# Performance work log

Measured on AMD Instinct MI355X. Metric: run time of the kernel, lower is better.

The kernel has to match this reference:

```python
import jax, jax.numpy as jnp
import numpy as np

N_NODES = 4096
M_NODES = 8192
DIM = 256


def _symnorm(A):
    # D^{-1/2} A D^{-1/2} with eps, via row/col scaling (same math as diag matmuls)
    d = A.sum(axis=1) + 1e-5
    s = d ** -0.5
    return A * s[:, None] * s[None, :]


def _gat(A, X, W, a_src, a_dst, b):
    # Dense-form GATConv (PyG semantics): edges are nonzeros of A plus self loops.
    N = A.shape[0]
    H, F = a_src.shape
    Xp = (X @ W).reshape(N, H, F)                     # [N, H, F]
    src = jnp.einsum('nhf,hf->nh', Xp, a_src)         # score of source node j
    dst = jnp.einsum('nhf,hf->nh', Xp, a_dst)         # score of target node i
    logits = jax.nn.leaky_relu(dst[:, None, :] + src[None, :, :], negative_slope=0.2)  # [i, j, h]
    mask = (A != 0.0) | jnp.eye(N, dtype=bool)        # add_self_loops=True
    logits = jnp.where(mask[:, :, None], logits, -jnp.inf)
    alpha = jax.nn.softmax(logits, axis=1)            # softmax over neighbors j
    out = jnp.einsum('ijh,jhf->ihf', alpha, Xp).reshape(N, H * F) + b
    return out


def setup_inputs() -> dict:
    key = jax.random.key(0)
    ks = jax.random.split(key, 32)

    def p(i, shape, scale=0.05):
        return jax.random.normal(ks[i], shape, dtype=jnp.float32) * scale

    R = jax.random.normal(ks[0], (N_NODES, N_NODES), dtype=jnp.float32)
    A = jax.nn.relu((R + R.T) * 0.5)
    X = jax.random.normal(ks[1], (N_NODES, DIM), dtype=jnp.float32)
    return dict(
        A=A, X=X,
        # down GT0: GATConv(256, 128, heads=4) -> 512
        Wd0=p(2, (256, 512)), asd0=p(3, (4, 128)), add0=p(4, (4, 128)), bd0=p(5, (512,)),
        # down GT1: GATConv(512, 256, heads=4) -> 1024
        Wd1=p(6, (512, 1024)), asd1=p(7, (4, 256)), add1=p(8, (4, 256)), bd1=p(9, (1024,)),
        # pool projections (Linear(in, 1))
        wp0=p(10, (1, 512)), bp0=p(11, (1,)),
        wp1=p(12, (1, 1024)), bp1=p(13, (1,)),
        # bottom GT: GATConv(1024, 512, heads=2) -> 1024
        Wb=p(14, (1024, 1024)), asb=p(15, (2, 512)), adb=p(16, (2, 512)), bb=p(17, (1024,)),
        # up GT (reversed[0]): GATConv(1024, 128, heads=4) -> 512
        Wu0=p(18, (1024, 512)), asu0=p(19, (4, 128)), adu0=p(20, (4, 128)), bu0=p(21, (512,)),
        # up GT (reversed[1]): GATConv(512, 64, heads=4) -> 256
        Wu1=p(22, (512, 256)), asu1=p(23, (4, 64)), adu1=p(24, (4, 64)), bu1=p(25, (256,)),
        # upsampler Linear(n_nodes, m_nodes)
        Wup=p(26, (M_NODES, N_NODES)), bup=p(27, (M_NODES,)),
    )


def reference(A, X, Wd0, asd0, add0, bd0, Wd1, asd1, add1, bd1, wp0, bp0, wp1, bp1,
              Wb, asb, adb, bb, Wu0, asu0, adu0, bu0, Wu1, asu1, adu1, bu1, Wup, bup):
    N0 = A.shape[0]
    A0 = A + jnp.eye(N0, dtype=A.dtype)  # A_ = A + I (used throughout; normalized A is dead code)

    # ---- down level 0 ----
    X0 = jax.nn.relu(_gat(A0, X, Wd0, asd0, add0, bd0))            # [4096, 512]
    s0 = jax.nn.sigmoid(X0 @ wp0[0] + bp0[0])
    k0 = max(2, N0 // 2)                                            # int(0.5 * N)
    v0, idx0 = jax.lax.top_k(s0, k0)
    A1 = _symnorm(A0[idx0][:, idx0])                                # [2048, 2048]
    X1in = X0[idx0] * v0[:, None]

    # ---- down level 1 ----
    X1 = jax.nn.relu(_gat(A1, X1in, Wd1, asd1, add1, bd1))          # [2048, 1024]
    s1 = jax.nn.sigmoid(X1 @ wp1[0] + bp1[0])
    k1 = max(2, k0 // 2)
    v1, idx1 = jax.lax.top_k(s1, k1)
    A2 = _symnorm(A1[idx1][:, idx1])                                # [1024, 1024]
    X2in = X1[idx1] * v1[:, None]

    # ---- bottom ----
    Xb = jax.nn.relu(_gat(A2, X2in, Wb, asb, adb, bb))              # [1024, 1024]

    # ---- up level 0: unpool to level-1 graph ----
    h = jnp.zeros((k0, Xb.shape[1]), Xb.dtype).at[idx1].set(Xb)
    Xu0 = jax.nn.relu(_gat(A1, h, Wu0, asu0, adu0, bu0))            # [2048, 512]
    rec0 = jax.nn.relu(Xu0 @ Xu0.T)

    # ---- up level 1: unpool to original graph ----
    h = jnp.zeros((N0, Xu0.shape[1]), Xu0.dtype).at[idx0].set(Xu0)
    Xu1 = jax.nn.relu(_gat(A0, h, Wu1, asu1, adu1, bu1))            # [4096, 256]
    rec1 = jax.nn.relu(Xu1 @ Xu1.T)

    # ---- upsampler: Linear over node dim, softmax over feature dim, reconstruct adjacency ----
    Z = jax.nn.softmax(Wup @ Xu1 + bup[:, None], axis=1)            # [8192, 256]
    A_up = jax.nn.relu(Z @ Z.T)                                     # [8192, 8192]
    return (A_up, A0, A1, rec0, rec1)
```

## Files before the change

kernel.cpp:

```cpp
#include <hip/hip_runtime.h>
#include <math.h>


typedef short bf16x8 __attribute__((ext_vector_type(8)));
typedef float f32x4 __attribute__((ext_vector_type(4)));

static __device__ __forceinline__ float wave_sum64(float v) {
#pragma unroll
  for (int off = 32; off; off >>= 1) v += __shfl_down(v, off);
  return v;
}

static __device__ __forceinline__ unsigned short f2b(float x) {
  unsigned u = __float_as_uint(x);
  unsigned r = (u + 0x7fffu + ((u >> 16) & 1u)) >> 16;
  return (unsigned short)r;
}

static __device__ __forceinline__ float b2f(unsigned short h) {
  return __uint_as_float(((unsigned)h) << 16);
}

__global__ void k_add_eye(const float* __restrict__ A, float* __restrict__ O) {
  size_t i = ((size_t)blockIdx.x * 256 + threadIdx.x) * 4;
  size_t r = i >> 12, c = i & 4095;
  float4 v = *reinterpret_cast<const float4*>(&A[i]);
  if (r >= c && r < c + 4) ((float*)&v)[r - c] += 1.f;
  *reinterpret_cast<float4*>(&O[i]) = v;
}

__global__ void k_fill0(float* __restrict__ p, int n) {
  int stride = gridDim.x * 256;
  for (int i = blockIdx.x * 256 + threadIdx.x; i < n; i += stride) p[i] = 0.f;
}

__global__ void k_split3(const float* __restrict__ S, unsigned short* __restrict__ D,
                         size_t PS, int n) {
  int stride = gridDim.x * 1024;
  for (int i = (blockIdx.x * 256 + threadIdx.x) * 4; i < n; i += stride) {
    float4 v = *reinterpret_cast<const float4*>(&S[i]);
    float xv[4] = {v.x, v.y, v.z, v.w};
    unsigned short o1[4], o2[4], o3[4];
#pragma unroll
    for (int e = 0; e < 4; ++e) {
      float x = xv[e];
      unsigned short a = f2b(x);
      float r1 = x - b2f(a);
      unsigned short b = f2b(r1);
      float r2 = r1 - b2f(b);
      o1[e] = a; o2[e] = b; o3[e] = f2b(r2);
    }
    *reinterpret_cast<uint2*>(&D[i]) = *reinterpret_cast<const uint2*>(o1);
    *reinterpret_cast<uint2*>(&D[PS + i]) = *reinterpret_cast<const uint2*>(o2);
    *reinterpret_cast<uint2*>(&D[2 * PS + i]) = *reinterpret_cast<const uint2*>(o3);
  }
}

__global__ void k_gather_scale_split3(const float* __restrict__ Xs, int Dd,
    const int* __restrict__ idx, const float* __restrict__ v,
    unsigned short* __restrict__ D, size_t PS) {
  int i = blockIdx.y;
  int f = (blockIdx.x * 256 + threadIdx.x) * 4;
  if (f >= Dd) return;
  float vi = v[i];
  float4 x4 = *reinterpret_cast<const float4*>(&Xs[(size_t)idx[i] * Dd + f]);
  float xv[4] = {x4.x * vi, x4.y * vi, x4.z * vi, x4.w * vi};
  unsigned short o1[4], o2[4], o3[4];
#pragma unroll
  for (int e = 0; e < 4; ++e) {
    float x = xv[e];
    unsigned short a = f2b(x);
    float r1 = x - b2f(a);
    unsigned short b = f2b(r1);
    float r2 = r1 - b2f(b);
    o1[e] = a; o2[e] = b; o3[e] = f2b(r2);
  }
  size_t e0 = (size_t)i * Dd + f;
  *reinterpret_cast<uint2*>(&D[e0]) = *reinterpret_cast<const uint2*>(o1);
  *reinterpret_cast<uint2*>(&D[PS + e0]) = *reinterpret_cast<const uint2*>(o2);
  *reinterpret_cast<uint2*>(&D[2 * PS + e0]) = *reinterpret_cast<const uint2*>(o3);
}

__global__ void k_gather_scale_b16(const float* __restrict__ Xs, int Dd,
    const int* __restrict__ idx, const float* __restrict__ v,
    unsigned short* __restrict__ D) {
  int i = blockIdx.y;
  int f = (blockIdx.x * 256 + threadIdx.x) * 4;
  if (f >= Dd) return;
  float vi = v[i];
  float4 x4 = *reinterpret_cast<const float4*>(&Xs[(size_t)idx[i] * Dd + f]);
  unsigned short o[4] = {f2b(x4.x * vi), f2b(x4.y * vi), f2b(x4.z * vi), f2b(x4.w * vi)};
  *reinterpret_cast<uint2*>(&D[(size_t)i * Dd + f]) = *reinterpret_cast<const uint2*>(o);
}

__global__ __launch_bounds__(256) void k_transpose_bf16(const float* __restrict__ S, int ldS,
    unsigned short* __restrict__ D, int R, int Cc) {
  __shared__ unsigned short T[64][72];
  int r0 = blockIdx.y << 6, c0 = blockIdx.x << 6;
  int tid = threadIdx.x;
  int tr = tid >> 4, tc4 = (tid & 15) << 2;
#pragma unroll
  for (int q = 0; q < 4; ++q) {
    int row = tr + q * 16;
    float4 v = *reinterpret_cast<const float4*>(&S[(size_t)(r0 + row) * ldS + c0 + tc4]);
    T[tc4 + 0][row] = f2b(v.x);
    T[tc4 + 1][row] = f2b(v.y);
    T[tc4 + 2][row] = f2b(v.z);
    T[tc4 + 3][row] = f2b(v.w);
  }
  __syncthreads();
#pragma unroll
  for (int q = 0; q < 4; ++q) {
    int row = tr + q * 16;
    *reinterpret_cast<uint2*>(&D[(size_t)(c0 + row) * R + r0 + tc4]) =
        *reinterpret_cast<const uint2*>(&T[row][tc4]);
  }
}

__global__ __launch_bounds__(256) void k_transpose_bb(const unsigned short* __restrict__ S,
    int ldS, unsigned short* __restrict__ D, int R, int Cc) {
  __shared__ unsigned short T[64][72];
  int r0 = blockIdx.y << 6, c0 = blockIdx.x << 6;
  int tid = threadIdx.x;
  int tr = tid >> 4, tc4 = (tid & 15) << 2;
#pragma unroll
  for (int q = 0; q < 4; ++q) {
    int row = tr + q * 16;
    uint2 v = *reinterpret_cast<const uint2*>(&S[(size_t)(r0 + row) * ldS + c0 + tc4]);
    const unsigned short* p = (const unsigned short*)&v;
    T[tc4 + 0][row] = p[0]; T[tc4 + 1][row] = p[1];
    T[tc4 + 2][row] = p[2]; T[tc4 + 3][row] = p[3];
  }
  __syncthreads();
#pragma unroll
  for (int q = 0; q < 4; ++q) {
    int row = tr + q * 16;
    *reinterpret_cast<uint2*>(&D[(size_t)(c0 + row) * R + r0 + tc4]) =
        *reinterpret_cast<const uint2*>(&T[row][tc4]);
  }
}

__global__ __launch_bounds__(256) void k_transpose_bf16h(const float* __restrict__ S, int ldS,
    int F, unsigned short* __restrict__ D, int R) {
  __shared__ unsigned short T[64][72];
  int h = blockIdx.z;
  int r0 = blockIdx.y << 6, c0 = blockIdx.x << 6;
  int tid = threadIdx.x;
  int tr = tid >> 4, tc4 = (tid & 15) << 2;
#pragma unroll
  for (int q = 0; q < 4; ++q) {
    int row = tr + q * 16;
    float4 v = *reinterpret_cast<const float4*>(&S[(size_t)(r0 + row) * ldS + h * F + c0 + tc4]);
    T[tc4 + 0][row] = f2b(v.x);
    T[tc4 + 1][row] = f2b(v.y);
    T[tc4 + 2][row] = f2b(v.z);
    T[tc4 + 3][row] = f2b(v.w);
  }
  __syncthreads();
#pragma unroll
  for (int q = 0; q < 4; ++q) {
    int row = tr + q * 16;
    *reinterpret_cast<uint2*>(&D[((size_t)h * F + c0 + row) * R + r0 + tc4]) =
        *reinterpret_cast<const uint2*>(&T[row][tc4]);
  }
}

__global__ __launch_bounds__(256) void k_transpose_split(const float* __restrict__ S, int ldS,
    int F, unsigned short* __restrict__ D, int R, size_t PS) {
  __shared__ unsigned short T[3][64][72];
  int h = blockIdx.z;
  int c0 = blockIdx.x << 6, r0 = blockIdx.y << 6;
  int tid = threadIdx.x;
  int tr = tid >> 4, tc4 = (tid & 15) << 2;
#pragma unroll
  for (int q = 0; q < 4; ++q) {
    int row = tr + q * 16;
    float4 v = *reinterpret_cast<const float4*>(&S[(size_t)(r0 + row) * ldS + h * F + c0 + tc4]);
    float xv[4] = {v.x, v.y, v.z, v.w};
#pragma unroll
    for (int e = 0; e < 4; ++e) {
      float x = xv[e];
      unsigned short h1 = f2b(x);
      float r1 = x - b2f(h1);
      unsigned short h2 = f2b(r1);
      float r2 = r1 - b2f(h2);
      T[0][tc4 + e][row] = h1;
      T[1][tc4 + e][row] = h2;
      T[2][tc4 + e][row] = f2b(r2);
    }
  }
  __syncthreads();
#pragma unroll
  for (int p = 0; p < 3; ++p)
#pragma unroll
    for (int q = 0; q < 4; ++q) {
      int row = tr + q * 16;
      *reinterpret_cast<uint2*>(&D[p * PS + (size_t)(h * F + c0 + row) * R + r0 + tc4]) =
          *reinterpret_cast<const uint2*>(&T[p][row][tc4]);
    }
}

__global__ __launch_bounds__(256, 2) void k_gemm_x6_bt(const unsigned short* __restrict__ As,
    size_t APS, const unsigned short* __restrict__ BTs, size_t BPS, float* __restrict__ C,
    int M, int N, int K) {
  __shared__ __align__(16) unsigned short Ai[3][128 * 40];
  __shared__ __align__(16) unsigned short Bj[3][128 * 40];
  int tid = threadIdx.x;
  int m0 = blockIdx.y << 7, n0 = blockIdx.x << 7;
  int lane = tid & 63, w = tid >> 6;
  int lr = lane & 15, kb = lane >> 4;
  int wr = (w >> 1) << 6, wc = (w & 1) << 6;
  int sr = tid >> 1, sc = (tid & 1) << 4;
  f32x4 acc[4][4] = {};
  for (int k0 = 0; k0 < K; k0 += 32) {
    __syncthreads();
#pragma unroll
    for (int p = 0; p < 3; ++p) {
      const unsigned short* ga = &As[p * APS + (size_t)(m0 + sr) * K + k0 + sc];
      *reinterpret_cast<uint4*>(&Ai[p][sr * 40 + sc]) = *reinterpret_cast<const uint4*>(ga);
      *reinterpret_cast<uint4*>(&Ai[p][sr * 40 + sc + 8]) =
          *reinterpret_cast<const uint4*>(ga + 8);
      const unsigned short* gb = &BTs[p * BPS + (size_t)(n0 + sr) * K + k0 + sc];
      *reinterpret_cast<uint4*>(&Bj[p][sr * 40 + sc]) = *reinterpret_cast<const uint4*>(gb);
      *reinterpret_cast<uint4*>(&Bj[p][sr * 40 + sc + 8]) =
          *reinterpret_cast<const uint4*>(gb + 8);
    }
    __syncthreads();
    bf16x8 af[4][3], bf_[4][3];
#pragma unroll
    for (int m = 0; m < 4; ++m)
#pragma unroll
      for (int p = 0; p < 3; ++p)
        af[m][p] = *reinterpret_cast<const bf16x8*>(&Ai[p][(wr + m * 16 + lr) * 40 + kb * 8]);
#pragma unroll
    for (int n = 0; n < 4; ++n)
#pragma unroll
      for (int p = 0; p < 3; ++p)
        bf_[n][p] = *reinterpret_cast<const bf16x8*>(&Bj[p][(wc + n * 16 + lr) * 40 + kb * 8]);
#pragma unroll
    for (int m = 0; m < 4; ++m)
#pragma unroll
      for (int n = 0; n < 4; ++n) {
        acc[m][n] = __builtin_amdgcn_mfma_f32_16x16x32_bf16(af[m][0], bf_[n][0], acc[m][n], 0, 0, 0);
        acc[m][n] = __builtin_amdgcn_mfma_f32_16x16x32_bf16(af[m][0], bf_[n][1], acc[m][n], 0, 0, 0);
        acc[m][n] = __builtin_amdgcn_mfma_f32_16x16x32_bf16(af[m][1], bf_[n][0], acc[m][n], 0, 0, 0);
        acc[m][n] = __builtin_amdgcn_mfma_f32_16x16x32_bf16(af[m][0], bf_[n][2], acc[m][n], 0, 0, 0);
        acc[m][n] = __builtin_amdgcn_mfma_f32_16x16x32_bf16(af[m][2], bf_[n][0], acc[m][n], 0, 0, 0);
        acc[m][n] = __builtin_amdgcn_mfma_f32_16x16x32_bf16(af[m][1], bf_[n][1], acc[m][n], 0, 0, 0);
      }
  }
  int orow = m0 + wr + (lane >> 4) * 4;
  int ocol = n0 + wc + lr;
#pragma unroll
  for (int m = 0; m < 4; ++m)
#pragma unroll
    for (int n = 0; n < 4; ++n)
#pragma unroll
      for (int r = 0; r < 4; ++r)
        C[(size_t)(orow + m * 16 + r) * N + ocol + n * 16] = acc[m][n][r];
}

__global__ __launch_bounds__(512, 4) void k_gat_x6(const float* __restrict__ Adj, int N,
    const unsigned short* __restrict__ XpS, size_t PS,
    const float* __restrict__ src, const float* __restrict__ dst,
    float* __restrict__ P, float* __restrict__ dP, int HF, int Ffull, int FP, int jchunk) {
  __shared__ __align__(16) unsigned short wL[3][128 * 40];
  __shared__ __align__(16) unsigned short xL[3][128 * 40];
  __shared__ float dstL[128];
  __shared__ float srcL[32];
  int H = HF / Ffull;
  int h = blockIdx.x / FP;
  int fp = blockIdx.x % FP;
  int f0 = fp << 7;
  int i0 = blockIdx.y << 7;
  int jb0 = blockIdx.z * jchunk;
  int tid = threadIdx.x;
  int si = tid >> 2, sj8 = (tid & 3) << 3;
  int lane = tid & 63, w = tid >> 6;
  int lr = lane & 15, kb = lane >> 4;
  int fs = w << 4;
  if (tid < 128) dstL[tid] = dst[(i0 + tid) * H + h];
  float dsum = 0.f;
  f32x4 acc[8] = {};
  int ntiles = jchunk >> 5;
  const unsigned short* xbase = XpS + ((size_t)h * Ffull + f0) * N;
  for (int t = 0; t < ntiles; ++t) {
    int jb = jb0 + (t << 5);
    __syncthreads();
    if (tid < 32) srcL[tid] = src[(jb + tid) * H + h];
    {
      int frow = tid >> 2;
#pragma unroll
      for (int p = 0; p < 3; ++p)
        *reinterpret_cast<uint4*>(&xL[p][frow * 40 + sj8]) =
            *reinterpret_cast<const uint4*>(&xbase[p * PS + (size_t)frow * N + jb + sj8]);
    }
    float4 av0 = *reinterpret_cast<const float4*>(&Adj[(size_t)(i0 + si) * N + jb + sj8]);
    float4 av1 = *reinterpret_cast<const float4*>(&Adj[(size_t)(i0 + si) * N + jb + sj8 + 4]);
    __syncthreads();
    {
      int gi = i0 + si;
      float dq = dstL[si];
      const float* a0 = (const float*)&av0;
      const float* a1 = (const float*)&av1;
      unsigned short h1[8], h2[8], h3[8];
      float ds = 0.f;
#pragma unroll
      for (int e = 0; e < 8; ++e) {
        float a = e < 4 ? a0[e] : a1[e - 4];
        float wv = 0.f;
        if (a != 0.f || (jb + sj8 + e) == gi) {
          float tt = dq + srcL[sj8 + e];
          tt = tt >= 0.f ? tt : 0.2f * tt;
          wv = __expf(tt);
        }
        ds += wv;
        unsigned u1 = __float_as_uint(wv);
        h1[e] = (unsigned short)(u1 >> 16);
        float r1 = wv - __uint_as_float(u1 & 0xffff0000u);
        unsigned u2 = __float_as_uint(r1);
        h2[e] = (unsigned short)(u2 >> 16);
        float r2 = r1 - __uint_as_float(u2 & 0xffff0000u);
        h3[e] = (unsigned short)(__float_as_uint(r2) >> 16);
      }
      dsum += ds;
      *reinterpret_cast<uint4*>(&wL[0][si * 40 + sj8]) = *reinterpret_cast<const uint4*>(h1);
      *reinterpret_cast<uint4*>(&wL[1][si * 40 + sj8]) = *reinterpret_cast<const uint4*>(h2);
      *reinterpret_cast<uint4*>(&wL[2][si * 40 + sj8]) = *reinterpret_cast<const uint4*>(h3);
    }
    __syncthreads();
    bf16x8 bf_[3];
#pragma unroll
    for (int p = 0; p < 3; ++p)
      bf_[p] = *reinterpret_cast<const bf16x8*>(&xL[p][(fs + lr) * 40 + kb * 8]);
#pragma unroll
    for (int m = 0; m < 8; ++m) {
      bf16x8 af[3];
#pragma unroll
      for (int p = 0; p < 3; ++p)
        af[p] = *reinterpret_cast<const bf16x8*>(&wL[p][(m * 16 + lr) * 40 + kb * 8]);
      acc[m] = __builtin_amdgcn_mfma_f32_16x16x32_bf16(af[0], bf_[0], acc[m], 0, 0, 0);
      acc[m] = __builtin_amdgcn_mfma_f32_16x16x32_bf16(af[0], bf_[1], acc[m], 0, 0, 0);
      acc[m] = __builtin_amdgcn_mfma_f32_16x16x32_bf16(af[1], bf_[0], acc[m], 0, 0, 0);
      acc[m] = __builtin_amdgcn_mfma_f32_16x16x32_bf16(af[0], bf_[2], acc[m], 0, 0, 0);
      acc[m] = __builtin_amdgcn_mfma_f32_16x16x32_bf16(af[2], bf_[0], acc[m], 0, 0, 0);
      acc[m] = __builtin_amdgcn_mfma_f32_16x16x32_bf16(af[1], bf_[1], acc[m], 0, 0, 0);
    }
  }
  if (fp == 0) {
    float v = dsum;
    v += __shfl_xor(v, 1);
    v += __shfl_xor(v, 2);
    if ((tid & 3) == 0)
      dP[(size_t)blockIdx.z * N * H + (i0 + si) * H + h] = v;
  }
  float* Pc = P + (size_t)blockIdx.z * N * HF;
  int orow = i0 + (lane >> 4) * 4;
  int ocol = h * Ffull + f0 + fs + lr;
#pragma unroll
  for (int m = 0; m < 8; ++m)
#pragma unroll
    for (int r = 0; r < 4; ++r)
      Pc[(size_t)(orow + m * 16 + r) * HF + ocol] = acc[m][r];
}

template <int NS, int HEADS>
__global__ __launch_bounds__(512) void k_gat_b16(const float* __restrict__ Adj, int N,
    const unsigned short* __restrict__ XpT,
    const float* __restrict__ src, const float* __restrict__ dst,
    float* __restrict__ P, float* __restrict__ dP, int HF, int F, int jchunk) {
  constexpr int HFB = NS * 128;
  __shared__ __align__(16) unsigned short wL[HEADS][128 * 40];
  __shared__ __align__(16) unsigned short xL[HFB * 40];
  __shared__ float dstL[HEADS][128];
  __shared__ float srcL[HEADS][32];
  int H = HF / F;
  int hf0 = blockIdx.x * HFB;
  int h0 = hf0 / F;
  int i0 = blockIdx.y << 7;
  int jb0 = blockIdx.z * jchunk;
  int tid = threadIdx.x;
  int si = tid >> 2, sj8 = (tid & 3) << 3;
  int lane = tid & 63, w = tid >> 6;
  int lr = lane & 15, kb = lane >> 4;
  int fs = w * (NS * 16);
  int hw = (hf0 + fs) / F - h0;
  if (tid < HEADS * 128)
    dstL[tid >> 7][tid & 127] = dst[(i0 + (tid & 127)) * H + h0 + (tid >> 7)];
  float dsum[HEADS] = {};
  f32x4 acc[8][NS] = {};
  int ntiles = jchunk >> 5;
  for (int t = 0; t < ntiles; ++t) {
    int jb = jb0 + (t << 5);
    __syncthreads();
    if (tid < HEADS * 32) srcL[tid >> 5][tid & 31] = src[(jb + (tid & 31)) * H + h0 + (tid >> 5)];
#pragma unroll
    for (int base = 0; base < HFB; base += 128) {
      int row = base + (tid >> 2);
      *reinterpret_cast<uint4*>(&xL[row * 40 + sj8]) =
          *reinterpret_cast<const uint4*>(&XpT[(size_t)(hf0 + row) * N + jb + sj8]);
    }
    float4 av0 = *reinterpret_cast<const float4*>(&Adj[(size_t)(i0 + si) * N + jb + sj8]);
    float4 av1 = *reinterpret_cast<const float4*>(&Adj[(size_t)(i0 + si) * N + jb + sj8 + 4]);
    __syncthreads();
    {
      int gi = i0 + si;
      const float* a0 = (const float*)&av0;
      const float* a1 = (const float*)&av1;
#pragma unroll
      for (int hh = 0; hh < HEADS; ++hh) {
        float dq = dstL[hh][si];
        unsigned short wb[8];
        float ds = 0.f;
#pragma unroll
        for (int e = 0; e < 8; ++e) {
          float a = e < 4 ? a0[e] : a1[e - 4];
          float wv = 0.f;
          if (a != 0.f || (jb + sj8 + e) == gi) {
            float tt = dq + srcL[hh][sj8 + e];
            tt = tt >= 0.f ? tt : 0.2f * tt;
            wv = __expf(tt);
          }
          ds += wv;
          wb[e] = f2b(wv);
        }
        dsum[hh] += ds;
        *reinterpret_cast<uint4*>(&wL[hh][si * 40 + sj8]) =
            *reinterpret_cast<const uint4*>(wb);
      }
    }
    __syncthreads();
    bf16x8 bf_[NS];
#pragma unroll
    for (int n = 0; n < NS; ++n)
      bf_[n] = *reinterpret_cast<const bf16x8*>(&xL[(fs + n * 16 + lr) * 40 + kb * 8]);
#pragma unroll
    for (int m = 0; m < 8; ++m) {
      bf16x8 a = *reinterpret_cast<const bf16x8*>(&wL[hw][(m * 16 + lr) * 40 + kb * 8]);
#pragma unroll
      for (int n = 0; n < NS; ++n)
        acc[m][n] = __builtin_amdgcn_mfma_f32_16x16x32_bf16(a, bf_[n], acc[m][n], 0, 0, 0);
    }
  }
#pragma unroll
  for (int hh = 0; hh < HEADS; ++hh) {
    float v = dsum[hh];
    v += __shfl_xor(v, 1);
    v += __shfl_xor(v, 2);
    if ((tid & 3) == 0)
      dP[(size_t)blockIdx.z * N * H + (i0 + si) * H + h0 + hh] = v;
  }
  float* Pc = P + (size_t)blockIdx.z * N * HF;
  int orow = i0 + (lane >> 4) * 4;
  int ocol0 = hf0 + fs + lr;
#pragma unroll
  for (int m = 0; m < 8; ++m)
#pragma unroll
    for (int n = 0; n < NS; ++n)
#pragma unroll
      for (int r = 0; r < 4; ++r)
        Pc[(size_t)(orow + m * 16 + r) * HF + ocol0 + n * 16] = acc[m][n][r];
}

__global__ void k_gat_reduce(const float* __restrict__ P, int nch, size_t chstride,
    const float* __restrict__ dP, size_t dstride, const float* __restrict__ bias,
    float* __restrict__ Of, unsigned short* __restrict__ Ob, int HF, int F, int n_total) {
  int e = (blockIdx.x * 256 + threadIdx.x) * 4;
  if (e >= n_total) return;
  float4 s = *reinterpret_cast<const float4*>(&P[e]);
  for (int c = 1; c < nch; ++c) {
    float4 v = *reinterpret_cast<const float4*>(&P[c * chstride + e]);
    s.x += v.x; s.y += v.y; s.z += v.z; s.w += v.w;
  }
  int i = e / HF;
  int hf = e - i * HF;
  int h = hf / F;
  float den = 0.f;
  for (int c = 0; c < nch; ++c) den += dP[c * dstride + i * (HF / F) + h];
  float inv = 1.f / den;
  float4 bz = *reinterpret_cast<const float4*>(&bias[hf]);
  float4 o;
  o.x = fmaxf(fmaf(s.x, inv, bz.x), 0.f);
  o.y = fmaxf(fmaf(s.y, inv, bz.y), 0.f);
  o.z = fmaxf(fmaf(s.z, inv, bz.z), 0.f);
  o.w = fmaxf(fmaf(s.w, inv, bz.w), 0.f);
  if (Of) *reinterpret_cast<float4*>(&Of[e]) = o;
  if (Ob) {
    unsigned short ob[4] = {f2b(o.x), f2b(o.y), f2b(o.z), f2b(o.w)};
    *reinterpret_cast<uint2*>(&Ob[e]) = *reinterpret_cast<const uint2*>(ob);
  }
}

__global__ __launch_bounds__(256) void k_syrk_mfma(const unsigned short* __restrict__ G,
    int M, int Kd, float* __restrict__ C) {
  if (blockIdx.x < blockIdx.y) return;
  __shared__ __align__(16) unsigned short Ai[128 * 40];
  __shared__ __align__(16) unsigned short Bj[128 * 40];
  int tid = threadIdx.x;
  int i0 = blockIdx.y << 7, j0 = blockIdx.x << 7;
  int srow = tid >> 1, scol = (tid & 1) << 3;
  int lane = tid & 63, w = tid >> 6;
  int wr = (w >> 1) << 6, wc = (w & 1) << 6;
  int lr = lane & 15, kb = lane >> 4;
  f32x4 acc[4][4] = {};
  const unsigned short* gA = G + (size_t)i0 * Kd;
  const unsigned short* gB = G + (size_t)j0 * Kd;
  for (int k0 = 0; k0 < Kd; k0 += 32) {
    __syncthreads();
#pragma unroll
    for (int kk = 0; kk < 32; kk += 16) {
      *reinterpret_cast<uint4*>(&Ai[srow * 40 + scol + kk]) =
          *reinterpret_cast<const uint4*>(&gA[(size_t)srow * Kd + k0 + scol + kk]);
      *reinterpret_cast<uint4*>(&Bj[srow * 40 + scol + kk]) =
          *reinterpret_cast<const uint4*>(&gB[(size_t)srow * Kd + k0 + scol + kk]);
    }
    __syncthreads();
    bf16x8 a[4], b[4];
#pragma unroll
    for (int m = 0; m < 4; ++m)
      a[m] = *reinterpret_cast<const bf16x8*>(&Ai[(wr + m * 16 + lr) * 40 + kb * 8]);
#pragma unroll
    for (int n = 0; n < 4; ++n)
      b[n] = *reinterpret_cast<const bf16x8*>(&Bj[(wc + n * 16 + lr) * 40 + kb * 8]);
#pragma unroll
    for (int m = 0; m < 4; ++m)
#pragma unroll
      for (int n = 0; n < 4; ++n)
        acc[m][n] = __builtin_amdgcn_mfma_f32_16x16x32_bf16(a[m], b[n], acc[m][n], 0, 0, 0);
  }
  int orow = i0 + wr + (lane >> 4) * 4;
  int ocol = j0 + wc + (lane & 15);
  bool mirror = (j0 != i0);
#pragma unroll
  for (int m = 0; m < 4; ++m)
#pragma unroll
    for (int n = 0; n < 4; ++n) {
      float4 v;
      v.x = fmaxf(acc[m][n][0], 0.f);
      v.y = fmaxf(acc[m][n][1], 0.f);
      v.z = fmaxf(acc[m][n][2], 0.f);
      v.w = fmaxf(acc[m][n][3], 0.f);
#pragma unroll
      for (int r = 0; r < 4; ++r)
        C[(size_t)(orow + m * 16 + r) * M + ocol + n * 16] = ((const float*)&v)[r];
      if (mirror)
        *reinterpret_cast<float4*>(
            &C[(size_t)(j0 + wc + n * 16 + lr) * M + i0 + wr + m * 16 + (lane >> 4) * 4]) = v;
    }
}

__global__ __launch_bounds__(256) void k_gemm_mfma_bt(const unsigned short* __restrict__ Amat,
    const unsigned short* __restrict__ BT, const float* __restrict__ bias,
    float* __restrict__ C, int M, int N, int Kd) {
  __shared__ __align__(16) unsigned short Ai[128 * 40];
  __shared__ __align__(16) unsigned short Bj[128 * 40];
  int tid = threadIdx.x;
  int m0 = blockIdx.y << 7, n0 = blockIdx.x << 7;
  int srow = tid >> 1, scol = (tid & 1) << 3;
  int lane = tid & 63, w = tid >> 6;
  int wr = (w >> 1) << 6, wc = (w & 1) << 6;
  int lr = lane & 15, kb = lane >> 4;
  f32x4 acc[4][4] = {};
  const unsigned short* gA = Amat + (size_t)m0 * Kd;
  const unsigned short* gB = BT + (size_t)n0 * Kd;
  for (int k0 = 0; k0 < Kd; k0 += 32) {
    __syncthreads();
#pragma unroll
    for (int kk = 0; kk < 32; kk += 16) {
      *reinterpret_cast<uint4*>(&Ai[srow * 40 + scol + kk]) =
          *reinterpret_cast<const uint4*>(&gA[(size_t)srow * Kd + k0 + scol + kk]);
      *reinterpret_cast<uint4*>(&Bj[srow * 40 + scol + kk]) =
          *reinterpret_cast<const uint4*>(&gB[(size_t)srow * Kd + k0 + scol + kk]);
    }
    __syncthreads();
    bf16x8 a[4], b[4];
#pragma unroll
    for (int m = 0; m < 4; ++m)
      a[m] = *reinterpret_cast<const bf16x8*>(&Ai[(wr + m * 16 + lr) * 40 + kb * 8]);
#pragma unroll
    for (int n = 0; n < 4; ++n)
      b[n] = *reinterpret_cast<const bf16x8*>(&Bj[(wc + n * 16 + lr) * 40 + kb * 8]);
#pragma unroll
    for (int m = 0; m < 4; ++m)
#pragma unroll
      for (int n = 0; n < 4; ++n)
        acc[m][n] = __builtin_amdgcn_mfma_f32_16x16x32_bf16(a[m], b[n], acc[m][n], 0, 0, 0);
  }
  int orow = m0 + wr + (lane >> 4) * 4;
  int ocol = n0 + wc + (lane & 15);
#pragma unroll
  for (int m = 0; m < 4; ++m)
#pragma unroll
    for (int n = 0; n < 4; ++n)
#pragma unroll
      for (int r = 0; r < 4; ++r) {
        float rb = bias ? bias[orow + m * 16 + r] : 0.f;
        C[(size_t)(orow + m * 16 + r) * N + ocol + n * 16] = acc[m][n][r] + rb;
      }
}

__global__ __launch_bounds__(512) void k_gemm_aup(const float* __restrict__ Wg,
    const unsigned short* __restrict__ BT, float* __restrict__ Pz, int Mtot, int Ktot,
    int kc_len) {
  __shared__ __align__(16) unsigned short Ai[128 * 40];
  __shared__ __align__(16) unsigned short Bj[256 * 40];
  int tid = threadIdx.x;
  int m0 = blockIdx.y << 7;
  int k0base = blockIdx.x * kc_len;
  int lane = tid & 63, w = tid >> 6;
  int wr = (w >> 2) << 6, wc = (w & 3) << 6;
  int lr = lane & 15, kb = lane >> 4;
  int ar = tid >> 2, ac8 = (tid & 3) << 3;
  int br = tid >> 1, bc16 = (tid & 1) << 4;
  f32x4 acc[4][4] = {};
  for (int kk = 0; kk < kc_len; kk += 32) {
    int k0 = k0base + kk;
    __syncthreads();
    {
      const float* arow = &Wg[(size_t)(m0 + ar) * Ktot + k0 + ac8];
      float4 v0 = *reinterpret_cast<const float4*>(arow);
      float4 v1 = *reinterpret_cast<const float4*>(arow + 4);
      unsigned short t8[8] = {f2b(v0.x), f2b(v0.y), f2b(v0.z), f2b(v0.w),
                              f2b(v1.x), f2b(v1.y), f2b(v1.z), f2b(v1.w)};
      *reinterpret_cast<uint4*>(&Ai[ar * 40 + ac8]) = *reinterpret_cast<const uint4*>(t8);
      const unsigned short* brow = &BT[(size_t)br * Ktot + k0 + bc16];
      *reinterpret_cast<uint4*>(&Bj[br * 40 + bc16]) = *reinterpret_cast<const uint4*>(brow);
      *reinterpret_cast<uint4*>(&Bj[br * 40 + bc16 + 8]) =
          *reinterpret_cast<const uint4*>(brow + 8);
    }
    __syncthreads();
    bf16x8 a[4], b[4];
#pragma unroll
    for (int m = 0; m < 4; ++m)
      a[m] = *reinterpret_cast<const bf16x8*>(&Ai[(wr + m * 16 + lr) * 40 + kb * 8]);
#pragma unroll
    for (int n = 0; n < 4; ++n)
      b[n] = *reinterpret_cast<const bf16x8*>(&Bj[(wc + n * 16 + lr) * 40 + kb * 8]);
#pragma unroll
    for (int m = 0; m < 4; ++m)
#pragma unroll
      for (int n = 0; n < 4; ++n)
        acc[m][n] = __builtin_amdgcn_mfma_f32_16x16x32_bf16(a[m], b[n], acc[m][n], 0, 0, 0);
  }
  float* outp = Pz + (size_t)blockIdx.x * Mtot * 256;
  int orow = m0 + wr + (lane >> 4) * 4;
  int ocol = wc + (lane & 15);
#pragma unroll
  for (int m = 0; m < 4; ++m)
#pragma unroll
    for (int n = 0; n < 4; ++n)
#pragma unroll
      for (int r = 0; r < 4; ++r)
        outp[(size_t)(orow + m * 16 + r) * 256 + ocol + n * 16] = acc[m][n][r];
}

__global__ __launch_bounds__(256) void k_softmax_fuse(const float* __restrict__ Pz, int nch,
    size_t chstride, const float* __restrict__ bias, unsigned short* __restrict__ ZB) {
  int row = blockIdx.x, tid = threadIdx.x;
  size_t e = (size_t)row * 256 + tid;
  float x = bias[row];
  for (int c = 0; c < nch; ++c) x += Pz[c * chstride + e];
  float m = x;
#pragma unroll
  for (int off = 32; off; off >>= 1) m = fmaxf(m, __shfl_down(m, off));
  __shared__ float red[4];
  __shared__ float bm, bs;
  if ((tid & 63) == 0) red[tid >> 6] = m;
  __syncthreads();
  if (tid == 0) bm = fmaxf(fmaxf(red[0], red[1]), fmaxf(red[2], red[3]));
  __syncthreads();
  float ev = expf(x - bm);
  float sm = wave_sum64(ev);
  __syncthreads();
  if ((tid & 63) == 0) red[tid >> 6] = sm;
  __syncthreads();
  if (tid == 0) bs = red[0] + red[1] + red[2] + red[3];
  __syncthreads();
  ZB[e] = f2b(ev / bs);
}

__global__ void k_src_dst(const float* __restrict__ Xp, const float* __restrict__ a_src,
    const float* __restrict__ a_dst, float* __restrict__ src, float* __restrict__ dst,
    int H, int F) {
  int n = blockIdx.x;
  int h = threadIdx.x >> 6, lane = threadIdx.x & 63;
  const float* x = Xp + ((size_t)n * H + h) * F;
  const float* as = a_src + h * F;
  const float* ad = a_dst + h * F;
  float ps = 0.f, pd = 0.f;
  for (int f = lane; f < F; f += 64) {
    float xv = x[f];
    ps = fmaf(xv, as[f], ps);
    pd = fmaf(xv, ad[f], pd);
  }
  ps = wave_sum64(ps);
  pd = wave_sum64(pd);
  if (lane == 0) { src[n * H + h] = ps; dst[n * H + h] = pd; }
}

__global__ __launch_bounds__(256) void k_score(const float* __restrict__ Xf,
    const float* __restrict__ wv, const float* __restrict__ bsc, float* __restrict__ s, int D) {
  int row = blockIdx.x * 4 + (threadIdx.x >> 6);
  int lane = threadIdx.x & 63;
  const float* x = Xf + (size_t)row * D;
  float p = 0.f;
  for (int f = lane; f < D; f += 64) p = fmaf(x[f], wv[f], p);
  p = wave_sum64(p);
  if (lane == 0) s[row] = 1.f / (1.f + expf(-(p + bsc[0])));
}

__global__ __launch_bounds__(256) void k_topk_rank(const float* __restrict__ s, int n, int k,
    int* __restrict__ idx, float* __restrict__ vals, float* __restrict__ mask) {
  extern __shared__ unsigned long long keys[];
  int tid = threadIdx.x;
  int i = blockIdx.x * 256 + tid;
  if (mask) mask[i] = 0.f;
  for (int j = tid; j < n; j += 256) {
    unsigned u = __float_as_uint(s[j]);
    unsigned ord = (u & 0x80000000u) ? ~u : (u | 0x80000000u);
    keys[j] = ((unsigned long long)ord << 32) | (unsigned)(~j);
  }
  __syncthreads();
  unsigned long long mykey = keys[i];
  int rank = 0;
#pragma unroll 4
  for (int j = 0; j < n; ++j) rank += (keys[j] > mykey);
  if (rank < k) {
    idx[rank] = i;
    vals[rank] = s[i];
    if (mask) mask[i] = 1.f;
  }
}

__global__ __launch_bounds__(256) void k_rowsum_mask(const float* __restrict__ A0, int N,
    const int* __restrict__ idx, const float* __restrict__ m, float* __restrict__ sv) {
  int i = blockIdx.x, tid = threadIdx.x;
  const float* row = A0 + (size_t)idx[i] * N;
  float p = 0.f;
  for (int j = tid * 4; j < N; j += 1024) {
    float4 a = *reinterpret_cast<const float4*>(&row[j]);
    float4 b = *reinterpret_cast<const float4*>(&m[j]);
    p += a.x * b.x + a.y * b.y + a.z * b.z + a.w * b.w;
  }
  p = wave_sum64(p);
  __shared__ float red[4];
  if ((tid & 63) == 0) red[tid >> 6] = p;
  __syncthreads();
  if (tid == 0) sv[i] = rsqrtf(red[0] + red[1] + red[2] + red[3] + 1e-5f);
}

__global__ __launch_bounds__(256) void k_gatherT(const float* __restrict__ A0, int N,
    const int* __restrict__ idx, float* __restrict__ T1, int k) {
  __shared__ float T[64][65];
  int i0 = blockIdx.x << 6, c0 = blockIdx.y << 6;
  int tid = threadIdx.x;
  int tr = tid >> 4, tc4 = (tid & 15) << 2;
#pragma unroll
  for (int q = 0; q < 4; ++q) {
    int row = tr + q * 16;
    float4 v = *reinterpret_cast<const float4*>(&A0[(size_t)idx[i0 + row] * N + c0 + tc4]);
    T[tc4 + 0][row] = v.x; T[tc4 + 1][row] = v.y; T[tc4 + 2][row] = v.z; T[tc4 + 3][row] = v.w;
  }
  __syncthreads();
#pragma unroll
  for (int q = 0; q < 4; ++q) {
    int row = tr + q * 16;
    float4 o;
    o.x = T[row][tc4]; o.y = T[row][tc4 + 1]; o.z = T[row][tc4 + 2]; o.w = T[row][tc4 + 3];
    *reinterpret_cast<float4*>(&T1[(size_t)(c0 + row) * k + i0 + tc4]) = o;
  }
}

__global__ void k_scaleT(const float* __restrict__ T1, int k, const int* __restrict__ idx,
    const float* __restrict__ sv, float* __restrict__ A1) {
  int j = blockIdx.y;
  int i = (blockIdx.x * 256 + threadIdx.x) * 4;
  float sj = sv[j];
  const float* r = T1 + (size_t)idx[j] * k;
  float4 v = *reinterpret_cast<const float4*>(&r[i]);
  float4 s = *reinterpret_cast<const float4*>(&sv[i]);
  v.x *= sj * s.x; v.y *= sj * s.y; v.z *= sj * s.z; v.w *= sj * s.w;
  *reinterpret_cast<float4*>(&A1[(size_t)j * k + i]) = v;
}

__global__ void k_gather_mat(const float* __restrict__ Asrc, int lda,
    const int* __restrict__ idx, float* __restrict__ B, int k) {
  int j = blockIdx.x * 256 + threadIdx.x;
  int i = blockIdx.y;
  B[(size_t)i * k + j] = Asrc[(size_t)idx[i] * lda + idx[j]];
}

__global__ void k_scatter_rows(const float* __restrict__ P, int D, const int* __restrict__ idx,
                               float* __restrict__ Xo) {
  int f = blockIdx.x * 256 + threadIdx.x;
  int i = blockIdx.y;
  Xo[(size_t)idx[i] * D + f] = P[(size_t)i * D + f];
}

extern "C" void kernel_launch(void* const* d_in, const int* in_sizes, int n_in,
                              void* d_out, int out_size, void* d_ws, size_t ws_size,
                              hipStream_t stream) {
  const float* A    = (const float*)d_in[0];
  const float* X    = (const float*)d_in[1];
  const float* Wd0  = (const float*)d_in[2];
  const float* asd0 = (const float*)d_in[3];
  const float* add0 = (const float*)d_in[4];
  const float* bd0  = (const float*)d_in[5];
  const float* Wd1  = (const float*)d_in[6];
  const float* asd1 = (const float*)d_in[7];
  const float* add1 = (const float*)d_in[8];
  const float* bd1  = (const float*)d_in[9];
  const float* wp0  = (const float*)d_in[10];
  const float* bp0  = (const float*)d_in[11];
  const float* wp1  = (const float*)d_in[12];
  const float* bp1  = (const float*)d_in[13];
  const float* Wb   = (const float*)d_in[14];
  const float* asb  = (const float*)d_in[15];
  const float* adb  = (const float*)d_in[16];
  const float* bb   = (const float*)d_in[17];
  const float* Wu0  = (const float*)d_in[18];
  const float* asu0 = (const float*)d_in[19];
  const float* adu0 = (const float*)d_in[20];
  const float* bu0  = (const float*)d_in[21];
  const float* Wu1  = (const float*)d_in[22];
  const float* asu1 = (const float*)d_in[23];
  const float* adu1 = (const float*)d_in[24];
  const float* bu1  = (const float*)d_in[25];
  const float* Wup  = (const float*)d_in[26];
  const float* bup  = (const float*)d_in[27];
  (void)in_sizes; (void)n_in; (void)out_size; (void)ws_size;

  float* out  = (float*)d_out;
  float* Aup  = out;
  float* A0   = out + 67108864ULL;
  float* A1   = A0 + 16777216ULL;
  float* rec0 = A1 + 4194304ULL;
  float* rec1 = rec0 + 4194304ULL;

  float* S = Aup;
  size_t off = 0;
  auto nxt = [&](size_t n) { float* p = S + off; off += (n + 1023) & ~(size_t)1023; return p; };
  float* Xp0  = nxt(4096 * 512);
  float* X0   = nxt(4096 * 512);
  float* src0 = nxt(4096 * 4);
  float* dst0 = nxt(4096 * 4);
  float* sc0  = nxt(4096);
  int*   idx0 = (int*)nxt(2048);
  float* v0   = nxt(2048);
  float* sv0  = nxt(2048);
  float* maskv = nxt(4096);
  float* Xp1  = nxt(2048 * 1024);
  float* X1   = nxt(2048 * 1024);
  float* src1 = nxt(2048 * 4);
  float* dst1 = nxt(2048 * 4);
  float* sc1  = nxt(2048);
  int*   idx1 = (int*)nxt(1024);
  float* v1   = nxt(1024);
  float* A2m  = nxt(1024 * 1024);
  float* Xpb  = nxt(1024 * 1024);
  float* srcb = nxt(1024 * 2);
  float* dstb = nxt(1024 * 2);
  float* Pu0  = nxt(1024 * 512);
  float* Xpu0 = nxt(2048 * 512);
  float* su0  = nxt(2048 * 4);
  float* du0  = nxt(2048 * 4);
  float* Pu1  = nxt(2048 * 256);
  float* Xpu1 = nxt(4096 * 256);
  float* su1  = nxt(4096 * 4);
  float* du1  = nxt(4096 * 4);
  float* dPp  = nxt(8 * 4096 * 4);
  float* P    = nxt((size_t)8 * 4096 * 512);
  float* T1   = nxt((size_t)4096 * 2048);
  unsigned short* XpS  = (unsigned short*)nxt(3200000);
  unsigned short* XSp  = (unsigned short*)nxt(1572864);
  unsigned short* Wd0T = (unsigned short*)nxt(196608);
  unsigned short* Wd1T = (unsigned short*)nxt(786432);
  unsigned short* XpT  = (unsigned short*)nxt(524288);
  unsigned short* X2inB = (unsigned short*)nxt(524288);
  unsigned short* XbB   = (unsigned short*)nxt(524288);
  unsigned short* WbT   = (unsigned short*)nxt(524288);
  unsigned short* Wu0T  = (unsigned short*)nxt(262144);
  unsigned short* Wu1T  = (unsigned short*)nxt(65536);

  float* W = (float*)d_ws;
  unsigned short* Xu1B = (unsigned short*)(W + 1048576);
  unsigned short* Xu0B = (unsigned short*)(W + 1048576 + 524288);

  float* Pz = rec1;
  unsigned short* ZB = (unsigned short*)(rec1 + 4 * 2097152);
  unsigned short* Xu1T = (unsigned short*)(rec1 + 4 * 2097152 + 1048576);

  const size_t PS0 = (size_t)4 * 128 * 4096;
  const size_t PS1 = (size_t)4 * 256 * 2048;

  k_add_eye<<<16384, 256, 0, stream>>>(A, A0);

  k_split3<<<1024, 256, 0, stream>>>(X, XSp, (size_t)4096 * 256, 4096 * 256);
  k_transpose_split<<<dim3(8, 4, 1), 256, 0, stream>>>(Wd0, 512, 512, Wd0T, 256,
                                                       (size_t)512 * 256);
  k_gemm_x6_bt<<<dim3(4, 32), 256, 0, stream>>>(XSp, (size_t)4096 * 256, Wd0T,
                                                (size_t)512 * 256, Xp0, 4096, 512, 256);
  k_src_dst<<<4096, 256, 0, stream>>>(Xp0, asd0, add0, src0, dst0, 4, 128);
  k_transpose_split<<<dim3(2, 64, 4), 256, 0, stream>>>(Xp0, 512, 128, XpS, 4096, PS0);
  k_gat_x6<<<dim3(4, 32, 4), 512, 0, stream>>>(A0, 4096, XpS, PS0, src0, dst0, P, dPp, 512,
                                               128, 1, 1024);
  k_gat_reduce<<<2048, 256, 0, stream>>>(P, 4, (size_t)4096 * 512, dPp, (size_t)4096 * 4, bd0,
                                         X0, nullptr, 512, 128, 4096 * 512);
  k_score<<<1024, 256, 0, stream>>>(X0, wp0, bp0, sc0, 512);
  k_topk_rank<<<16, 256, 4096 * 8, stream>>>(sc0, 4096, 2048, idx0, v0, maskv);
  k_rowsum_mask<<<2048, 256, 0, stream>>>(A0, 4096, idx0, maskv, sv0);
  k_gatherT<<<dim3(32, 64), 256, 0, stream>>>(A0, 4096, idx0, T1, 2048);
  k_scaleT<<<dim3(2, 2048), 256, 0, stream>>>(T1, 2048, idx0, sv0, A1);

  k_gather_scale_split3<<<dim3(1, 2048), 256, 0, stream>>>(X0, 512, idx0, v0, XSp,
                                                           (size_t)2048 * 512);
  k_transpose_split<<<dim3(16, 8, 1), 256, 0, stream>>>(Wd1, 1024, 1024, Wd1T, 512,
                                                        (size_t)1024 * 512);
  k_gemm_x6_bt<<<dim3(8, 16), 256, 0, stream>>>(XSp, (size_t)2048 * 512, Wd1T,
                                                (size_t)1024 * 512, Xp1, 2048, 1024, 512);
  k_src_dst<<<2048, 256, 0, stream>>>(Xp1, asd1, add1, src1, dst1, 4, 256);
  k_transpose_split<<<dim3(4, 32, 4), 256, 0, stream>>>(Xp1, 1024, 256, XpS, 2048, PS1);
  k_gat_x6<<<dim3(8, 16, 4), 512, 0, stream>>>(A1, 2048, XpS, PS1, src1, dst1, P, dPp, 1024,
                                               256, 2, 512);
  k_gat_reduce<<<2048, 256, 0, stream>>>(P, 4, (size_t)2048 * 1024, dPp, (size_t)2048 * 4, bd1,
                                         X1, nullptr, 1024, 256, 2048 * 1024);
  k_score<<<512, 256, 0, stream>>>(X1, wp1, bp1, sc1, 1024);
  k_topk_rank<<<8, 256, 2048 * 8, stream>>>(sc1, 2048, 1024, idx1, v1, nullptr);
  k_gather_mat<<<dim3(4, 1024), 256, 0, stream>>>(A1, 2048, idx1, A2m, 1024);
  k_gather_scale_b16<<<dim3(1, 1024), 256, 0, stream>>>(X1, 1024, idx1, v1, X2inB);

  k_transpose_bf16<<<dim3(16, 16), 256, 0, stream>>>(Wb, 1024, WbT, 1024, 1024);
  k_gemm_mfma_bt<<<dim3(8, 8), 256, 0, stream>>>(X2inB, WbT, nullptr, Xpb, 1024, 1024, 1024);
  k_src_dst<<<1024, 128, 0, stream>>>(Xpb, asb, adb, srcb, dstb, 2, 512);
  k_transpose_bf16h<<<dim3(8, 16, 2), 256, 0, stream>>>(Xpb, 1024, 512, XpT, 1024);
  k_gat_b16<4, 1><<<dim3(2, 8, 4), 512, 0, stream>>>(A2m, 1024, XpT, srcb, dstb, P, dPp, 1024,
                                                     512, 256);
  k_gat_reduce<<<1024, 256, 0, stream>>>(P, 4, (size_t)1024 * 1024, dPp, (size_t)1024 * 2, bb,
                                         nullptr, XbB, 1024, 512, 1024 * 1024);

  k_transpose_bf16<<<dim3(8, 16), 256, 0, stream>>>(Wu0, 512, Wu0T, 1024, 512);
  k_gemm_mfma_bt<<<dim3(4, 8), 256, 0, stream>>>(XbB, Wu0T, nullptr, Pu0, 1024, 512, 1024);
  k_fill0<<<1024, 256, 0, stream>>>(Xpu0, 2048 * 512);
  k_scatter_rows<<<dim3(2, 1024), 256, 0, stream>>>(Pu0, 512, idx1, Xpu0);
  k_src_dst<<<2048, 256, 0, stream>>>(Xpu0, asu0, adu0, su0, du0, 4, 128);
  k_transpose_bf16h<<<dim3(2, 32, 4), 256, 0, stream>>>(Xpu0, 512, 128, XpT, 2048);
  k_gat_b16<4, 4><<<dim3(1, 16, 8), 512, 0, stream>>>(A1, 2048, XpT, su0, du0, P, dPp, 512,
                                                      128, 256);
  k_gat_reduce<<<1024, 256, 0, stream>>>(P, 8, (size_t)2048 * 512, dPp, (size_t)2048 * 4, bu0,
                                         nullptr, Xu0B, 512, 128, 2048 * 512);

  k_transpose_bf16<<<dim3(4, 8), 256, 0, stream>>>(Wu1, 256, Wu1T, 512, 256);
  k_gemm_mfma_bt<<<dim3(2, 16), 256, 0, stream>>>(Xu0B, Wu1T, nullptr, Pu1, 2048, 256, 512);
  k_fill0<<<1024, 256, 0, stream>>>(Xpu1, 4096 * 256);
  k_scatter_rows<<<dim3(1, 2048), 256, 0, stream>>>(Pu1, 256, idx0, Xpu1);
  k_src_dst<<<4096, 256, 0, stream>>>(Xpu1, asu1, adu1, su1, du1, 4, 64);
  k_transpose_bf16h<<<dim3(1, 64, 4), 256, 0, stream>>>(Xpu1, 256, 64, XpT, 4096);
  k_gat_b16<2, 4><<<dim3(1, 32, 8), 512, 0, stream>>>(A0, 4096, XpT, su1, du1, P, dPp, 256,
                                                      64, 512);
  k_gat_reduce<<<1024, 256, 0, stream>>>(P, 8, (size_t)4096 * 256, dPp, (size_t)4096 * 4, bu1,
                                         nullptr, Xu1B, 256, 64, 4096 * 256);
  k_transpose_bb<<<dim3(4, 64), 256, 0, stream>>>(Xu1B, 256, Xu1T, 4096, 256);

  k_gemm_aup<<<dim3(4, 64), 512, 0, stream>>>(Wup, Xu1T, Pz, 8192, 4096, 1024);
  k_softmax_fuse<<<8192, 256, 0, stream>>>(Pz, 4, (size_t)8192 * 256, bup, ZB);
  k_syrk_mfma<<<dim3(64, 64), 256, 0, stream>>>(ZB, 8192, 256, Aup);

  k_syrk_mfma<<<dim3(32, 32), 256, 0, stream>>>(Xu1B, 4096, 256, rec1);
  k_syrk_mfma<<<dim3(16, 16), 256, 0, stream>>>(Xu0B, 2048, 512, rec0);
}
```

Baseline: 960.9 us.

## Replace fill+scatter unpool with inverse-index gather and double split-K for upsampler GEMM

Top-k now writes an inverse index (rank+1 or 0) per node. Unpooling becomes a single gather kernel, replacing a zero-fill plus scatter. The masked rowsum uses the inverse index instead of a float mask. The upsampler GEMM split-K factor goes from 4 to 8, with softmax reducing 8 partials, and ZB/Xu1T move into the workspace so the larger Pz partial buffer fits. This saves launches and a memory pass, and gives the GEMM more parallelism in exchange for more partial-sum traffic.

After: 941.2 us. -2.0%, faster.

```diff
diff --git a/kernel.cpp b/kernel.cpp
--- a/kernel.cpp
+++ b/kernel.cpp
@@ -27,11 +27,6 @@
   float4 v = *reinterpret_cast<const float4*>(&A[i]);
   if (r >= c && r < c + 4) ((float*)&v)[r - c] += 1.f;
   *reinterpret_cast<float4*>(&O[i]) = v;
-}
-
-__global__ void k_fill0(float* __restrict__ p, int n) {
-  int stride = gridDim.x * 256;
-  for (int i = blockIdx.x * 256 + threadIdx.x; i < n; i += stride) p[i] = 0.f;
 }
 
 __global__ void k_split3(const float* __restrict__ S, unsigned short* __restrict__ D,
@@ -710,11 +705,10 @@
 }
 
 __global__ __launch_bounds__(256) void k_topk_rank(const float* __restrict__ s, int n, int k,
-    int* __restrict__ idx, float* __restrict__ vals, float* __restrict__ mask) {
+    int* __restrict__ idx, float* __restrict__ vals, int* __restrict__ inv) {
   extern __shared__ unsigned long long keys[];
   int tid = threadIdx.x;
   int i = blockIdx.x * 256 + tid;
-  if (mask) mask[i] = 0.f;
   for (int j = tid; j < n; j += 256) {
     unsigned u = __float_as_uint(s[j]);
     unsigned ord = (u & 0x80000000u) ? ~u : (u | 0x80000000u);
@@ -725,22 +719,26 @@
   int rank = 0;
 #pragma unroll 4
   for (int j = 0; j < n; ++j) rank += (keys[j] > mykey);
-  if (rank < k) {
+  int sel = rank < k;
+  inv[i] = sel ? rank + 1 : 0;
+  if (sel) {
     idx[rank] = i;
     vals[rank] = s[i];
-    if (mask) mask[i] = 1.f;
   }
 }
 
 __global__ __launch_bounds__(256) void k_rowsum_mask(const float* __restrict__ A0, int N,
-    const int* __restrict__ idx, const float* __restrict__ m, float* __restrict__ sv) {
+    const int* __restrict__ idx, const int* __restrict__ inv, float* __restrict__ sv) {
   int i = blockIdx.x, tid = threadIdx.x;
   const float* row = A0 + (size_t)idx[i] * N;
   float p = 0.f;
   for (int j = tid * 4; j < N; j += 1024) {
     float4 a = *reinterpret_cast<const float4*>(&row[j]);
-    float4 b = *reinterpret_cast<const float4*>(&m[j]);
-    p += a.x * b.x + a.y * b.y + a.z * b.z + a.w * b.w;
+    int4 b = *reinterpret_cast<const int4*>(&inv[j]);
+    if (b.x) p += a.x;
+    if (b.y) p += a.y;
+    if (b.z) p += a.z;
+    if (b.w) p += a.w;
   }
   p = wave_sum64(p);
   __shared__ float red[4];
@@ -790,11 +788,12 @@
   B[(size_t)i * k + j] = Asrc[(size_t)idx[i] * lda + idx[j]];
 }
 
-__global__ void k_scatter_rows(const float* __restrict__ P, int D, const int* __restrict__ idx,
-                               float* __restrict__ Xo) {
+__global__ void k_unpool(const float* __restrict__ Pn, int Dd, const int* __restrict__ inv,
+                         float* __restrict__ Xo) {
+  int node = blockIdx.y;
   int f = blockIdx.x * 256 + threadIdx.x;
-  int i = blockIdx.y;
-  Xo[(size_t)idx[i] * D + f] = P[(size_t)i * D + f];
+  int r = inv[node];
+  Xo[(size_t)node * Dd + f] = r ? Pn[(size_t)(r - 1) * Dd + f] : 0.f;
 }
 
 extern "C" void kernel_launch(void* const* d_in, const int* in_sizes, int n_in,
@@ -848,7 +847,7 @@
   int*   idx0 = (int*)nxt(2048);
   float* v0   = nxt(2048);
   float* sv0  = nxt(2048);
-  float* maskv = nxt(4096);
+  int*   inv0 = (int*)nxt(4096);
   float* Xp1  = nxt(2048 * 1024);
   float* X1   = nxt(2048 * 1024);
   float* src1 = nxt(2048 * 4);
@@ -856,6 +855,7 @@
   float* sc1  = nxt(2048);
   int*   idx1 = (int*)nxt(1024);
   float* v1   = nxt(1024);
+  int*   inv1 = (int*)nxt(2048);
   float* A2m  = nxt(1024 * 1024);
   float* Xpb  = nxt(1024 * 1024);
   float* srcb = nxt(1024 * 2);
@@ -882,16 +882,15 @@
   unsigned short* Wu0T  = (unsigned short*)nxt(262144);
   unsigned short* Wu1T  = (unsigned short*)nxt(65536);
 
-  float* W = (float*)d_ws;
-  unsigned short* Xu1B = (unsigned short*)(W + 1048576);
-  unsigned short* Xu0B = (unsigned short*)(W + 1048576 + 524288);
+  unsigned short* Xu1B = (unsigned short*)d_ws;
+  unsigned short* Xu0B = (unsigned short*)((char*)d_ws + (2 << 20));
+  unsigned short* ZB   = (unsigned short*)((char*)d_ws + (4 << 20));
+  unsigned short* Xu1T = (unsigned short*)((char*)d_ws + (8 << 20));
 
   float* Pz = rec1;
-  unsigned short* ZB = (unsigned short*)(rec1 + 4 * 2097152);
-  unsigned short* Xu1T = (unsigned short*)(rec1 + 4 * 2097152 + 1048576);
-
-  const size_t PS0 = (size_t)4 * 128 * 4096;
-  const size_t PS1 = (size_t)4 * 256 * 2048;
+
+  const size_t PS0 = (size_t)512 * 4096;
+  const size_t PS1 = (size_t)1024 * 2048;
 
   k_add_eye<<<16384, 256, 0, stream>>>(A, A0);
 
@@ -907,8 +906,8 @@
   k_gat_reduce<<<2048, 256, 0, stream>>>(P, 4, (size_t)4096 * 512, dPp, (size_t)4096 * 4, bd0,
                                          X0, nullptr, 512, 128, 4096 * 512);
   k_score<<<1024, 256, 0, stream>>>(X0, wp0, bp0, sc0, 512);
-  k_topk_rank<<<16, 256, 4096 * 8, stream>>>(sc0, 4096, 2048, idx0, v0, maskv);
-  k_rowsum_mask<<<2048, 256, 0, stream>>>(A0, 4096, idx0, maskv, sv0);
+  k_topk_rank<<<16, 256, 4096 * 8, stream>>>(sc0, 4096, 2048, idx0, v0, inv0);
+  k_rowsum_mask<<<2048, 256, 0, stream>>>(A0, 4096, idx0, inv0, sv0);
   k_gatherT<<<dim3(32, 64), 256, 0, stream>>>(A0, 4096, idx0, T1, 2048);
   k_scaleT<<<dim3(2, 2048), 256, 0, stream>>>(T1, 2048, idx0, sv0, A1);
 
@@ -925,7 +924,7 @@
   k_gat_reduce<<<2048, 256, 0, stream>>>(P, 4, (size_t)2048 * 1024, dPp, (size_t)2048 * 4, bd1,
                                          X1, nullptr, 1024, 256, 2048 * 1024);
   k_score<<<512, 256, 0, stream>>>(X1, wp1, bp1, sc1, 1024);
-  k_topk_rank<<<8, 256, 2048 * 8, stream>>>(sc1, 2048, 1024, idx1, v1, nullptr);
+  k_topk_rank<<<8, 256, 2048 * 8, stream>>>(sc1, 2048, 1024, idx1, v1, inv1);
   k_gather_mat<<<dim3(4, 1024), 256, 0, stream>>>(A1, 2048, idx1, A2m, 1024);
   k_gather_scale_b16<<<dim3(1, 1024), 256, 0, stream>>>(X1, 1024, idx1, v1, X2inB);
 
@@ -940,8 +939,7 @@
 
   k_transpose_bf16<<<dim3(8, 16), 256, 0, stream>>>(Wu0, 512, Wu0T, 1024, 512);
   k_gemm_mfma_bt<<<dim3(4, 8), 256, 0, stream>>>(XbB, Wu0T, nullptr, Pu0, 1024, 512, 1024);
-  k_fill0<<<1024, 256, 0, stream>>>(Xpu0, 2048 * 512);
-  k_scatter_rows<<<dim3(2, 1024), 256, 0, stream>>>(Pu0, 512, idx1, Xpu0);
+  k_unpool<<<dim3(2, 2048), 256, 0, stream>>>(Pu0, 512, inv1, Xpu0);
   k_src_dst<<<2048, 256, 0, stream>>>(Xpu0, asu0, adu0, su0, du0, 4, 128);
   k_transpose_bf16h<<<dim3(2, 32, 4), 256, 0, stream>>>(Xpu0, 512, 128, XpT, 2048);
   k_gat_b16<4, 4><<<dim3(1, 16, 8), 512, 0, stream>>>(A1, 2048, XpT, su0, du0, P, dPp, 512,
@@ -951,8 +949,7 @@
 
   k_transpose_bf16<<<dim3(4, 8), 256, 0, stream>>>(Wu1, 256, Wu1T, 512, 256);
   k_gemm_mfma_bt<<<dim3(2, 16), 256, 0, stream>>>(Xu0B, Wu1T, nullptr, Pu1, 2048, 256, 512);
-  k_fill0<<<1024, 256, 0, stream>>>(Xpu1, 4096 * 256);
-  k_scatter_rows<<<dim3(1, 2048), 256, 0, stream>>>(Pu1, 256, idx0, Xpu1);
+  k_unpool<<<dim3(1, 4096), 256, 0, stream>>>(Pu1, 256, inv0, Xpu1);
   k_src_dst<<<4096, 256, 0, stream>>>(Xpu1, asu1, adu1, su1, du1, 4, 64);
   k_transpose_bf16h<<<dim3(1, 64, 4), 256, 0, stream>>>(Xpu1, 256, 64, XpT, 4096);
   k_gat_b16<2, 4><<<dim3(1, 32, 8), 512, 0, stream>>>(A0, 4096, XpT, su1, du1, P, dPp, 256,
@@ -961,8 +958,8 @@
                                          nullptr, Xu1B, 256, 64, 4096 * 256);
   k_transpose_bb<<<dim3(4, 64), 256, 0, stream>>>(Xu1B, 256, Xu1T, 4096, 256);
 
-  k_gemm_aup<<<dim3(4, 64), 512, 0, stream>>>(Wup, Xu1T, Pz, 8192, 4096, 1024);
-  k_softmax_fuse<<<8192, 256, 0, stream>>>(Pz, 4, (size_t)8192 * 256, bup, ZB);
+  k_gemm_aup<<<dim3(8, 64), 512, 0, stream>>>(Wup, Xu1T, Pz, 8192, 4096, 512);
+  k_softmax_fuse<<<8192, 256, 0, stream>>>(Pz, 8, (size_t)8192 * 256, bup, ZB);
   k_syrk_mfma<<<dim3(64, 64), 256, 0, stream>>>(ZB, 8192, 256, Aup);
 
   k_syrk_mfma<<<dim3(32, 32), 256, 0, stream>>>(Xu1B, 4096, 256, rec1);
```
